# Kernel tuning notes

Measured on AMD Instinct MI355X. Metric: run time of the kernel, lower is better.

Reference implementation:

```python
import jax, jax.numpy as jnp
import numpy as np

L = 28          # layers
D = 1024        # hidden
HQ = 16         # query heads
HKV = 8         # kv heads
HD = 128        # head dim
DFF = 3072      # mlp intermediate
Q = 512         # prefill length (= end_step, past_kv_len = 0)
EPS = 1e-6


def setup_inputs() -> dict:
    key = jax.random.key(0)
    ks = jax.random.split(key, 12)
    s = 0.02
    hidden_states = jax.random.normal(ks[0], (1, Q, D), jnp.float32)
    # RoPE tables (concatenated-halves layout, base 1e6 as in Qwen3)
    pos = jnp.arange(Q, dtype=jnp.float32)
    inv_freq = 1.0 / (1e6 ** (jnp.arange(0, HD, 2, dtype=jnp.float32) / HD))
    freqs = pos[:, None] * inv_freq[None, :]              # [Q, HD/2]
    emb = jnp.concatenate([freqs, freqs], axis=-1)        # [Q, HD]
    position_cos = jnp.cos(emb)[None]                     # [1, Q, HD]
    position_sin = jnp.sin(emb)[None]
    # causal mask: 0 where key_pos <= query_pos else -1e9 ; [1,1,Q,Q]
    i = jnp.arange(Q)
    attention_mask = jnp.where(i[None, :] <= i[:, None], 0.0, -1e9).astype(jnp.float32)[None, None]
    # stacked per-layer weights (torch Linear y = x @ W^T stored here as [in,out])
    Wq = jax.random.normal(ks[1], (L, D, HQ * HD), jnp.float32) * s
    Wk = jax.random.normal(ks[2], (L, D, HKV * HD), jnp.float32) * s
    Wv = jax.random.normal(ks[3], (L, D, HKV * HD), jnp.float32) * s
    Wo = jax.random.normal(ks[4], (L, HQ * HD, D), jnp.float32) * s
    Wg = jax.random.normal(ks[5], (L, D, DFF), jnp.float32) * s
    Wu = jax.random.normal(ks[6], (L, D, DFF), jnp.float32) * s
    Wd = jax.random.normal(ks[7], (L, DFF, D), jnp.float32) * s
    ln1 = jnp.ones((L, D), jnp.float32)
    ln2 = jnp.ones((L, D), jnp.float32)
    qn = jnp.ones((L, HD), jnp.float32)
    kn = jnp.ones((L, HD), jnp.float32)
    return {"hidden_states": hidden_states, "position_cos": position_cos,
            "position_sin": position_sin, "attention_mask": attention_mask,
            "Wq": Wq, "Wk": Wk, "Wv": Wv, "Wo": Wo, "Wg": Wg, "Wu": Wu, "Wd": Wd,
            "ln1": ln1, "ln2": ln2, "qn": qn, "kn": kn}


def rmsnorm(x, w):
    return x * jax.lax.rsqrt(jnp.mean(x * x, axis=-1, keepdims=True) + EPS) * w


def rotate_half(x):
    x1, x2 = jnp.split(x, 2, axis=-1)
    return jnp.concatenate([-x2, x1], axis=-1)


def reference(hidden_states, position_cos, position_sin, attention_mask,
              Wq, Wk, Wv, Wo, Wg, Wu, Wd, ln1, ln2, qn, kn):
    q_len = hidden_states.shape[1]
    scale = 1.0 / np.sqrt(HD)
    cos = position_cos[:, None]   # [1,1,Q,HD] broadcast over heads
    sin = position_sin[:, None]

    def layer(h, p):
        wq, wk, wv, wo, wg, wu, wd, l1, l2, qw, kw = p
        x = rmsnorm(h, l1)
        q = (x @ wq).reshape(1, q_len, HQ, HD).transpose(0, 2, 1, 3)   # [1,HQ,Q,HD]
        k = (x @ wk).reshape(1, q_len, HKV, HD).transpose(0, 2, 1, 3)  # [1,HKV,Q,HD]
        v = (x @ wv).reshape(1, q_len, HKV, HD).transpose(0, 2, 1, 3)
        q = rmsnorm(q, qw)
        k = rmsnorm(k, kw)
        q = q * cos + rotate_half(q) * sin
        k = k * cos + rotate_half(k) * sin
        # fp16 KV-cache round trip (faithful to k.half() store / .float() load)
        k = k.astype(jnp.float16).astype(jnp.float32)
        v = v.astype(jnp.float16).astype(jnp.float32)
        # GQA: repeat kv heads
        k = jnp.repeat(k, HQ // HKV, axis=1)
        v = jnp.repeat(v, HQ // HKV, axis=1)
        scores = jnp.einsum('bhqd,bhkd->bhqk', q, k) * scale + attention_mask
        probs = jax.nn.softmax(scores, axis=-1)
        attn = jnp.einsum('bhqk,bhkd->bhqd', probs, v)
        attn = attn.transpose(0, 2, 1, 3).reshape(1, q_len, HQ * HD)
        h = h + attn @ wo
        y = rmsnorm(h, l2)
        h = h + (jax.nn.silu(y @ wg) * (y @ wu)) @ wd
        return h, None

    params = (Wq, Wk, Wv, Wo, Wg, Wu, Wd, ln1, ln2, qn, kn)
    out, _ = jax.lax.scan(layer, hidden_states, params)
    return out
```

## Files before the change

### kernel.cpp

```cpp
#include <hip/hip_runtime.h>
#include <stdint.h>


typedef __bf16 bf16_t;
typedef _Float16 f16_t;
typedef __bf16 bf16x8 __attribute__((ext_vector_type(8)));
typedef __bf16 bf16x4 __attribute__((ext_vector_type(4)));
typedef _Float16 f16x8 __attribute__((ext_vector_type(8)));
typedef float f32x4 __attribute__((ext_vector_type(4)));

#define SEQ 512
#define HD 128

#define IMG_QKV 0ull
#define IMG_WO  8388608ull
#define IMG_GU  12582912ull
#define IMG_WD  25165824ull
#define IMG_LAYER_BYTES 31457280ull

typedef const __attribute__((address_space(1))) uint32_t as1_u32;
typedef __attribute__((address_space(3))) uint32_t as3_u32;

__device__ __forceinline__ void gload16(const void* g, void* l) {
    __builtin_amdgcn_global_load_lds((as1_u32*)g, (as3_u32*)l, 16, 0, 0);
}

#define WAITV12 asm volatile("s_waitcnt vmcnt(12)" ::: "memory")
#define WAITV6  asm volatile("s_waitcnt vmcnt(6)" ::: "memory")
#define WAITV0  asm volatile("s_waitcnt vmcnt(0)" ::: "memory")

__device__ __forceinline__ size_t aoff(int row, int col, int ldak) {
    return (((size_t)((row >> 6) * ldak + (col >> 6))) << 13) +
           ((size_t)(row & 63) << 7) +
           (size_t)((((col & 63) << 1)) ^ ((row & 7) << 4));
}

__global__ __launch_bounds__(256) void k_copy(const float* __restrict__ src,
                                              float* __restrict__ dst)
{
    size_t i = ((size_t)blockIdx.x * 256 + threadIdx.x) * 4;
    *(float4*)(dst + i) = *(const float4*)(src + i);
}

__device__ __forceinline__ void conv_tile(
    int b, int lay,
    const float* __restrict__ Wq, const float* __restrict__ Wk,
    const float* __restrict__ Wv, const float* __restrict__ Wo,
    const float* __restrict__ Wg, const float* __restrict__ Wu,
    const float* __restrict__ Wd, char* __restrict__ ib, void* smemv)
{
    const float* wq = Wq + (size_t)lay * 1024 * 2048;
    const float* wk = Wk + (size_t)lay * 1024 * 1024;
    const float* wv = Wv + (size_t)lay * 1024 * 1024;
    const float* wo = Wo + (size_t)lay * 2048 * 1024;
    const float* wg = Wg + (size_t)lay * 1024 * 3072;
    const float* wu = Wu + (size_t)lay * 1024 * 3072;
    const float* wd = Wd + (size_t)lay * 3072 * 1024;

    const float* src = nullptr;
    int ldbw = 0, n, kt, guMode = 0;
    size_t dstoff;
    if (b < 1024) {
        n = b >> 4; kt = b & 15;
        int C0 = n * 64;
        if (C0 < 2048)      { src = wq + C0;          ldbw = 2048; }
        else if (C0 < 3072) { src = wk + (C0 - 2048); ldbw = 1024; }
        else                { src = wv + (C0 - 3072); ldbw = 1024; }
        src += (size_t)(kt * 64) * ldbw;
        dstoff = IMG_QKV + (size_t)b * 8192;
    } else if (b < 1536) {
        int b2 = b - 1024; n = b2 >> 5; kt = b2 & 31;
        src = wo + (size_t)(kt * 64) * 1024 + n * 64; ldbw = 1024;
        dstoff = IMG_WO + (size_t)b2 * 8192;
    } else if (b < 3072) {
        int b3 = b - 1536; n = b3 >> 4; kt = b3 & 15;
        guMode = 1; ldbw = 3072;
        dstoff = IMG_GU + (size_t)b3 * 8192;
    } else {
        int b4 = b - 3072; n = b4 / 48; kt = b4 % 48;
        src = wd + (size_t)(kt * 64) * 1024 + n * 64; ldbw = 1024;
        dstoff = IMG_WD + (size_t)b4 * 8192;
    }

    float (*T)[68] = (float (*)[68])smemv;
    int tid = threadIdx.x;
    if (!guMode) {
#pragma unroll
        for (int it = 0; it < 4; ++it) {
            int idx = it * 256 + tid;
            int kk = idx >> 4, seg = idx & 15;
            *(float4*)&T[kk][seg * 4] = *(const float4*)(src + (size_t)kk * ldbw + seg * 4);
        }
    } else {
        const float* wg_ = wg + (size_t)(kt * 64) * 3072;
        const float* wu_ = wu + (size_t)(kt * 64) * 3072;
#pragma unroll
        for (int it = 0; it < 4; ++it) {
            int idx = it * 256 + tid;
            int kk = idx >> 4, seg = idx & 15;
            int nl = seg * 4;
            int colc = n * 32 + ((nl >> 5) & 1) * 16 + (nl & 15);
            const float* s2 = (((nl >> 4) & 1) ? wu_ : wg_) + (size_t)kk * 3072 + colc;
            *(float4*)&T[kk][nl] = *(const float4*)s2;
        }
    }
    __syncthreads();
    char* dst = ib + dstoff;
#pragma unroll
    for (int it = 0; it < 2; ++it) {
        int kg = tid & 7;
        int nrow = it * 32 + (tid >> 3);
        bf16x8 o;
#pragma unroll
        for (int j = 0; j < 8; ++j) o[j] = (bf16_t)T[kg * 8 + j][nrow];
        *(bf16x8*)(dst + nrow * 128 + ((kg * 16) ^ ((nrow & 7) << 4))) = o;
    }
}

__global__ __launch_bounds__(256) void k_conv(
    int lay,
    const float* __restrict__ Wq, const float* __restrict__ Wk,
    const float* __restrict__ Wv, const float* __restrict__ Wo,
    const float* __restrict__ Wg, const float* __restrict__ Wu,
    const float* __restrict__ Wd, char* __restrict__ img)
{
    __shared__ __align__(16) char smem[17408];
    conv_tile(blockIdx.x, lay, Wq, Wk, Wv, Wo, Wg, Wu, Wd, img, smem);
}

__global__ __launch_bounds__(256) void k_rms(
    float* __restrict__ h, const bf16_t* __restrict__ parts, int nparts,
    const float* __restrict__ w, char* __restrict__ ximg)
{
    int t = blockIdx.x, tid = threadIdx.x;
    size_t base = (size_t)t * 1024 + tid * 4;
    float4 v = *(const float4*)(h + base);
    for (int p = 0; p < nparts; ++p) {
        bf16x4 a = *(const bf16x4*)(parts + (size_t)p * 524288 + base);
        v.x += (float)a[0]; v.y += (float)a[1]; v.z += (float)a[2]; v.w += (float)a[3];
    }
    if (nparts) *(float4*)(h + base) = v;
    float ss = v.x * v.x + v.y * v.y + v.z * v.z + v.w * v.w;
#pragma unroll
    for (int m = 1; m < 64; m <<= 1) ss += __shfl_xor(ss, m);
    __shared__ float red[4];
    if ((tid & 63) == 0) red[tid >> 6] = ss;
    __syncthreads();
    float tot = (red[0] + red[1]) + (red[2] + red[3]);
    float sc = rsqrtf(tot * (1.0f / 1024.0f) + 1e-6f);
    float4 wv4 = *(const float4*)(w + tid * 4);
    bf16x4 o;
    o[0] = (bf16_t)(v.x * sc * wv4.x);
    o[1] = (bf16_t)(v.y * sc * wv4.y);
    o[2] = (bf16_t)(v.z * sc * wv4.z);
    o[3] = (bf16_t)(v.w * sc * wv4.w);
    *(bf16x4*)(ximg + aoff(t, tid * 4, 16)) = o;
}

__global__ __launch_bounds__(256) void k_finalize(
    const float* __restrict__ h, const bf16_t* __restrict__ parts,
    float* __restrict__ out)
{
    size_t base = ((size_t)blockIdx.x * 256 + threadIdx.x) * 4;
    float4 v = *(const float4*)(h + base);
#pragma unroll
    for (int p = 0; p < 4; ++p) {
        bf16x4 a = *(const bf16x4*)(parts + (size_t)p * 524288 + base);
        v.x += (float)a[0]; v.y += (float)a[1]; v.z += (float)a[2]; v.w += (float)a[3];
    }
    *(float4*)(out + base) = v;
}

template <int NBN, int SPLITK, int LDAK>
__device__ __forceinline__ void gemm_loop(
    const char* __restrict__ Aimg, const char* __restrict__ Bimg,
    char* smem, int f, f32x4 (&acc)[2][4], int& bmO, int& bnO, int& sO)
{
    const int steps = LDAK / SPLITK;
    int bm = f / (NBN * SPLITK);
    int r = f % (NBN * SPLITK);
    int s = r / NBN;
    int bn = r % NBN;
    int k0d = s * steps;
    bmO = bm; bnO = bn; sO = s;

    int tid = threadIdx.x;
    int wv = tid >> 6, l = tid & 63, lg = l >> 4, lr = l & 15;
    int wr = wv >> 1, wc = wv & 1;

#pragma unroll
    for (int i = 0; i < 2; ++i)
#pragma unroll
        for (int j = 0; j < 4; ++j) { f32x4 z = {0.f, 0.f, 0.f, 0.f}; acc[i][j] = z; }

    auto stage = [&](int buf, int kt) {
        const char* ab = Aimg + ((size_t)(bm * LDAK + k0d + kt)) * 8192;
        const char* b0 = Bimg + ((size_t)((2 * bn) * LDAK + k0d + kt)) * 8192;
        const char* b1 = Bimg + ((size_t)((2 * bn + 1) * LDAK + k0d + kt)) * 8192;
        char* al = smem + buf * 24576;
        char* bl = al + 8192;
#pragma unroll
        for (int u = 0; u < 2; ++u) {
            int off = (wv * 2 + u) * 1024;
            gload16(ab + off + l * 16, al + off);
        }
#pragma unroll
        for (int u = 0; u < 4; ++u) {
            int off = (wv * 4 + u) * 1024;
            const char* src = (off < 8192) ? (b0 + off) : (b1 + off - 8192);
            gload16(src + l * 16, bl + off);
        }
    };
    auto compute = [&](int buf) {
        const char* as = smem + buf * 24576;
        const char* bs = as + 8192 + wc * 8192;
        __builtin_amdgcn_s_setprio(1);
#pragma unroll
        for (int c = 0; c < 2; ++c) {
            int co = (c * 64 + lg * 16) ^ ((lr & 7) << 4);
            bf16x8 af[2], bf[4];
#pragma unroll
            for (int i = 0; i < 2; ++i)
                af[i] = *(const bf16x8*)(as + (wr * 32 + i * 16 + lr) * 128 + co);
#pragma unroll
            for (int j = 0; j < 4; ++j)
                bf[j] = *(const bf16x8*)(bs + (j * 16 + lr) * 128 + co);
#pragma unroll
            for (int i = 0; i < 2; ++i)
#pragma unroll
                for (int j = 0; j < 4; ++j)
                    acc[i][j] = __builtin_amdgcn_mfma_f32_16x16x32_bf16(
                        af[i], bf[j], acc[i][j], 0, 0, 0);
        }
        __builtin_amdgcn_s_setprio(0);
    };

    stage(0, 0);
    stage(1, 1);
    int buf = 0;
    for (int kt = 0; kt < steps; ++kt) {
        if (kt + 2 < steps)      { stage((kt + 2) % 3, kt + 2); WAITV12; }
        else if (kt + 1 < steps) { WAITV6; }
        else                     { WAITV0; }
        __builtin_amdgcn_sched_barrier(0);
        __builtin_amdgcn_s_barrier();
        __builtin_amdgcn_sched_barrier(0);
        compute(buf);
        __builtin_amdgcn_s_barrier();
        buf = (buf == 2) ? 0 : buf + 1;
    }
}

__global__ __launch_bounds__(256) void g_qkvf(
    const char* __restrict__ Aimg, const char* __restrict__ Bimg,
    const float* __restrict__ cosb, const float* __restrict__ sinb,
    const float* __restrict__ qw, const float* __restrict__ kw,
    f16_t* __restrict__ qf, f16_t* __restrict__ kf, f16_t* __restrict__ vT,
    const float* Wq, const float* Wk, const float* Wv, const float* Wo,
    const float* Wg, const float* Wu, const float* Wd,
    int lnext, char* __restrict__ imgnext)
{
    __shared__ __align__(128) char smem[73728];
    if (blockIdx.x >= 256) {
        conv_tile(blockIdx.x - 256, lnext, Wq, Wk, Wv, Wo, Wg, Wu, Wd, imgnext, smem);
        return;
    }
    f32x4 acc[2][4];
    int bm, bn, s;
    gemm_loop<32, 1, 16>(Aimg, Bimg, smem, blockIdx.x, acc, bm, bn, s);

    int tid = threadIdx.x;
    int wv = tid >> 6, l = tid & 63, lg = l >> 4, lr = l & 15;
    int wr = wv >> 1, wc = wv & 1;
    float (*X)[132] = (float (*)[132])smem;
    __syncthreads();
#pragma unroll
    for (int i = 0; i < 2; ++i)
#pragma unroll
        for (int j = 0; j < 4; ++j)
#pragma unroll
            for (int ii = 0; ii < 4; ++ii)
                X[wr * 32 + i * 16 + lg * 4 + ii][wc * 64 + j * 16 + lr] = acc[i][j][ii];
    __syncthreads();

    int t0 = bm * 64;
    if (bn < 24) {
        bool isq = bn < 16;
        int slot = isq ? bn : bn - 16;
        const float* wn = isq ? qw : kw;
        int r = tid >> 2, part = tid & 3;
        float ss = 0.f;
#pragma unroll
        for (int c = 0; c < 32; ++c) { float v = X[r][part * 32 + c]; ss += v * v; }
        ss += __shfl_xor(ss, 1);
        ss += __shfl_xor(ss, 2);
        float sc = rsqrtf(ss * (1.0f / 128.0f) + 1e-6f);
        int t = t0 + r;
        int d0 = part * 16;
        float o1v[16], o2v[16];
#pragma unroll
        for (int c = 0; c < 16; ++c) {
            int d = d0 + c;
            float xv1 = X[r][d] * sc * wn[d];
            float xv2 = X[r][d + 64] * sc * wn[d + 64];
            o1v[c] = xv1 * cosb[t * HD + d] - xv2 * sinb[t * HD + d];
            o2v[c] = xv2 * cosb[t * HD + d + 64] + xv1 * sinb[t * HD + d + 64];
        }
        f16x8 w0, w1, w2, w3;
#pragma unroll
        for (int c = 0; c < 8; ++c) {
            w0[c] = (f16_t)o1v[c];     w1[c] = (f16_t)o1v[8 + c];
            w2[c] = (f16_t)o2v[c];     w3[c] = (f16_t)o2v[8 + c];
        }
        f16_t* o = (isq ? qf : kf) + ((size_t)slot * SEQ + t) * HD;
        *(f16x8*)(o + d0) = w0;
        *(f16x8*)(o + d0 + 8) = w1;
        *(f16x8*)(o + d0 + 64) = w2;
        *(f16x8*)(o + d0 + 72) = w3;
    } else {
        int kvh = bn - 24;
#pragma unroll
        for (int it = 0; it < 4; ++it) {
            int task = it * 256 + tid;
            int d = task >> 3, seg = task & 7;
            f16x8 o;
#pragma unroll
            for (int j = 0; j < 8; ++j) o[j] = (f16_t)X[seg * 8 + j][d];
            *(f16x8*)(vT + ((size_t)kvh * HD + d) * SEQ + t0 + seg * 8) = o;
        }
    }
}

__global__ __launch_bounds__(256) void g_wo(
    const char* A, const char* B, bf16_t* parts,
    const float* Wq, const float* Wk, const float* Wv, const float* Wo,
    const float* Wg, const float* Wu, const float* Wd,
    int lnext, char* imgnext)
{
    __shared__ __align__(128) char smem[73728];
    if (blockIdx.x >= 256) {
        conv_tile(blockIdx.x - 256 + 960, lnext, Wq, Wk, Wv, Wo, Wg, Wu, Wd, imgnext, smem);
        return;
    }
    f32x4 acc[2][4];
    int bm, bn, s;
    gemm_loop<8, 4, 32>(A, B, smem, blockIdx.x, acc, bm, bn, s);
    int tid = threadIdx.x;
    int wv = tid >> 6, l = tid & 63, lg = l >> 4, lr = l & 15;
    int wr = wv >> 1, wc = wv & 1;
    bf16_t* P = parts + (size_t)s * 524288;
#pragma unroll
    for (int i = 0; i < 2; ++i)
#pragma unroll
        for (int j = 0; j < 4; ++j)
#pragma unroll
            for (int ii = 0; ii < 4; ++ii) {
                int row = bm * 64 + wr * 32 + i * 16 + lg * 4 + ii;
                int col = bn * 128 + wc * 64 + j * 16 + lr;
                P[(size_t)row * 1024 + col] = (bf16_t)acc[i][j][ii];
            }
}

__global__ __launch_bounds__(256) void g_gu(
    const char* A, const char* B, char* mimg,
    const float* Wq, const float* Wk, const float* Wv, const float* Wo,
    const float* Wg, const float* Wu, const float* Wd,
    int lnext, char* imgnext)
{
    __shared__ __align__(128) char smem[73728];
    if (blockIdx.x >= 384) {
        conv_tile(blockIdx.x - 384 + 1920, lnext, Wq, Wk, Wv, Wo, Wg, Wu, Wd, imgnext, smem);
        return;
    }
    f32x4 acc[2][4];
    int bm, bn, s;
    gemm_loop<48, 1, 16>(A, B, smem, blockIdx.x, acc, bm, bn, s);
    int tid = threadIdx.x;
    int wv = tid >> 6, l = tid & 63, lg = l >> 4, lr = l & 15;
    int wr = wv >> 1, wc = wv & 1;
#pragma unroll
    for (int i = 0; i < 2; ++i)
#pragma unroll
        for (int jp = 0; jp < 2; ++jp)
#pragma unroll
            for (int ii = 0; ii < 4; ++ii) {
                int row = bm * 64 + wr * 32 + i * 16 + lg * 4 + ii;
                int col = (bn * 2 + wc) * 32 + jp * 16 + lr;
                float gv = acc[i][2 * jp][ii];
                float uv = acc[i][2 * jp + 1][ii];
                float val = gv / (1.f + __expf(-gv)) * uv;
                *(bf16_t*)(mimg + aoff(row, col, 48)) = (bf16_t)val;
            }
}

__global__ __launch_bounds__(256) void k_wdc(
    const char* A, const char* B, bf16_t* parts,
    const float* Wq, const float* Wk, const float* Wv, const float* Wo,
    const float* Wg, const float* Wu, const float* Wd,
    int lnext, char* imgnext)
{
    __shared__ __align__(128) char smem[73728];
    int b = blockIdx.x;
    if (b >= 256) {
        conv_tile(b - 256 + 2880, lnext, Wq, Wk, Wv, Wo, Wg, Wu, Wd, imgnext, smem);
        return;
    }
    f32x4 acc[2][4];
    int bm, bn, s;
    gemm_loop<8, 4, 48>(A, B, smem, b, acc, bm, bn, s);
    int tid = threadIdx.x;
    int wv = tid >> 6, l = tid & 63, lg = l >> 4, lr = l & 15;
    int wr = wv >> 1, wc = wv & 1;
    bf16_t* P = parts + (size_t)s * 524288;
#pragma unroll
    for (int i = 0; i < 2; ++i)
#pragma unroll
        for (int j = 0; j < 4; ++j)
#pragma unroll
            for (int ii = 0; ii < 4; ++ii) {
                int row = bm * 64 + wr * 32 + i * 16 + lg * 4 + ii;
                int col = bn * 128 + wc * 64 + j * 16 + lr;
                P[(size_t)row * 1024 + col] = (bf16_t)acc[i][j][ii];
            }
}

__global__ __launch_bounds__(128) void k_attn(
    const f16_t* __restrict__ qf, const f16_t* __restrict__ kf,
    const f16_t* __restrict__ vT, char* __restrict__ attimg)
{
    int h = blockIdx.x >> 4, qb = 15 - (blockIdx.x & 15);
    int kvh = h >> 1;
    __shared__ f16_t Kt[64][136];
    __shared__ f16_t Vt[128][72];
    __shared__ f16_t Pl[2][16][72];
    int tid = threadIdx.x;
    int wv = tid >> 6, l = tid & 63, lg = l >> 4, lr = l & 15;
    int q0 = qb * 32;
    int qrow = q0 + wv * 16;

    f16x8 aq[4];
    const f16_t* qp = qf + ((size_t)h * SEQ + qrow + lr) * HD;
#pragma unroll
    for (int c = 0; c < 4; ++c) aq[c] = *(const f16x8*)(qp + c * 32 + lg * 8);

    f32x4 accv[8];
#pragma unroll
    for (int df = 0; df < 8; ++df) { f32x4 z = {0.f, 0.f, 0.f, 0.f}; accv[df] = z; }
    float mrun[4], lrun[4];
#pragma unroll
    for (int ii = 0; ii < 4; ++ii) { mrun[ii] = -3e38f; lrun[ii] = 0.f; }

    int ktiles = (q0 + 32 + 63) >> 6;
    for (int kt = 0; kt < ktiles; ++kt) {
        int kt0 = kt * 64;
        __syncthreads();
#pragma unroll
        for (int it = 0; it < 8; ++it) {
            int idx = it * 128 + tid;
            int r = idx >> 4, seg = idx & 15;
            *(int4*)&Kt[r][seg * 8] =
                *(const int4*)(kf + ((size_t)kvh * SEQ + kt0 + r) * HD + seg * 8);
        }
#pragma unroll
        for (int it = 0; it < 8; ++it) {
            int idx = it * 128 + tid;
            int r = idx >> 3, seg = idx & 7;
            *(int4*)&Vt[r][seg * 8] =
                *(const int4*)(vT + ((size_t)kvh * HD + r) * SEQ + kt0 + seg * 8);
        }
        __syncthreads();

        f32x4 s[4];
#pragma unroll
        for (int nf = 0; nf < 4; ++nf) {
            f32x4 a = {0.f, 0.f, 0.f, 0.f};
#pragma unroll
            for (int c = 0; c < 4; ++c) {
                f16x8 bk = *(const f16x8*)&Kt[nf * 16 + lr][c * 32 + lg * 8];
                a = __builtin_amdgcn_mfma_f32_16x16x32_f16(aq[c], bk, a, 0, 0, 0);
            }
            s[nf] = a;
        }
        const float scale = 0.08838834764831845f;
        float tmax[4] = {-3e38f, -3e38f, -3e38f, -3e38f};
#pragma unroll
        for (int nf = 0; nf < 4; ++nf) {
            int ktg = kt0 + nf * 16 + lr;
#pragma unroll
            for (int ii = 0; ii < 4; ++ii) {
                int qg = qrow + lg * 4 + ii;
                float vv = s[nf][ii] * scale;
                vv = (ktg <= qg) ? vv : -1e30f;
                s[nf][ii] = vv;
                tmax[ii] = fmaxf(tmax[ii], vv);
            }
        }
#pragma unroll
        for (int m = 1; m < 16; m <<= 1)
#pragma unroll
            for (int ii = 0; ii < 4; ++ii)
                tmax[ii] = fmaxf(tmax[ii], __shfl_xor(tmax[ii], m));
        float corr[4];
#pragma unroll
        for (int ii = 0; ii < 4; ++ii) {
            float mnew = fmaxf(mrun[ii], tmax[ii]);
            corr[ii] = __expf(mrun[ii] - mnew);
            mrun[ii] = mnew;
        }
        float tsum[4] = {0.f, 0.f, 0.f, 0.f};
#pragma unroll
        for (int nf = 0; nf < 4; ++nf)
#pragma unroll
            for (int ii = 0; ii < 4; ++ii) {
                float pp = __expf(s[nf][ii] - mrun[ii]);
                s[nf][ii] = pp;
                tsum[ii] += pp;
            }
#pragma unroll
        for (int m = 1; m < 16; m <<= 1)
#pragma unroll
            for (int ii = 0; ii < 4; ++ii) tsum[ii] += __shfl_xor(tsum[ii], m);
#pragma unroll
        for (int ii = 0; ii < 4; ++ii) lrun[ii] = lrun[ii] * corr[ii] + tsum[ii];
#pragma unroll
        for (int df = 0; df < 8; ++df)
#pragma unroll
            for (int ii = 0; ii < 4; ++ii) accv[df][ii] *= corr[ii];
#pragma unroll
        for (int nf = 0; nf < 4; ++nf)
#pragma unroll
            for (int ii = 0; ii < 4; ++ii)
                Pl[wv][lg * 4 + ii][nf * 16 + lr] = (f16_t)s[nf][ii];
        __syncthreads();
#pragma unroll
        for (int c = 0; c < 2; ++c) {
            f16x8 ap = *(const f16x8*)&Pl[wv][lr][c * 32 + lg * 8];
#pragma unroll
            for (int df = 0; df < 8; ++df) {
                f16x8 bv = *(const f16x8*)&Vt[df * 16 + lr][c * 32 + lg * 8];
                accv[df] = __builtin_amdgcn_mfma_f32_16x16x32_f16(ap, bv, accv[df], 0, 0, 0);
            }
        }
    }
#pragma unroll
    for (int df = 0; df < 8; ++df)
#pragma unroll
        for (int ii = 0; ii < 4; ++ii) {
            int qg = qrow + lg * 4 + ii;
            int col = h * HD + df * 16 + lr;
            *(bf16_t*)(attimg + aoff(qg, col, 32)) =
                (bf16_t)(accv[df][ii] / lrun[ii]);
        }
}

extern "C" void kernel_launch(void* const* d_in, const int* in_sizes, int n_in,
                              void* d_out, int out_size, void* d_ws, size_t ws_size,
                              hipStream_t stream)
{
    const float* hin  = (const float*)d_in[0];
    const float* cosb = (const float*)d_in[1];
    const float* sinb = (const float*)d_in[2];
    const float* Wq = (const float*)d_in[4];
    const float* Wk = (const float*)d_in[5];
    const float* Wv = (const float*)d_in[6];
    const float* Wo = (const float*)d_in[7];
    const float* Wg = (const float*)d_in[8];
    const float* Wu = (const float*)d_in[9];
    const float* Wd = (const float*)d_in[10];
    const float* Ln1 = (const float*)d_in[11];
    const float* Ln2 = (const float*)d_in[12];
    const float* Qn = (const float*)d_in[13];
    const float* Kn = (const float*)d_in[14];

    char* p = (char*)d_ws;
    auto alloc = [&](size_t bytes) { char* r = p; p += bytes; return r; };
    float*  h     = (float*)alloc(2097152);
    bf16_t* parts = (bf16_t*)alloc(4194304);
    char*   ximg  = alloc(1048576);
    char*   yimg  = alloc(1048576);
    char*   attimg= alloc(2097152);
    char*   mimg  = alloc(3145728);
    f16_t*  qf    = (f16_t*)alloc(2097152);
    f16_t*  kf    = (f16_t*)alloc(1048576);
    f16_t*  vT    = (f16_t*)alloc(1048576);
    char*   imgA  = alloc(IMG_LAYER_BYTES);
    size_t fixed = (size_t)(imgA + IMG_LAYER_BYTES - (char*)d_ws);
    bool pp = ws_size >= fixed + IMG_LAYER_BYTES;
    char* imgB = pp ? alloc(IMG_LAYER_BYTES) : imgA;

    k_copy<<<512, 256, 0, stream>>>(hin, h);
    k_conv<<<3840, 256, 0, stream>>>(0, Wq, Wk, Wv, Wo, Wg, Wu, Wd, imgA);

    for (int l = 0; l < 28; ++l) {
        char* img  = (l & 1) ? imgB : imgA;
        char* imgn = (l & 1) ? imgA : imgB;
        bool cv = pp && (l < 27);
        int ln = l + 1;

        k_rms<<<512, 256, 0, stream>>>(h, parts, l == 0 ? 0 : 4,
                                       Ln1 + (size_t)l * 1024, ximg);
        g_qkvf<<<cv ? 1216 : 256, 256, 0, stream>>>(
            ximg, img + IMG_QKV, cosb, sinb,
            Qn + (size_t)l * 128, Kn + (size_t)l * 128, qf, kf, vT,
            Wq, Wk, Wv, Wo, Wg, Wu, Wd, ln, imgn);
        k_attn<<<256, 128, 0, stream>>>(qf, kf, vT, attimg);
        g_wo<<<cv ? 1216 : 256, 256, 0, stream>>>(
            attimg, img + IMG_WO, parts,
            Wq, Wk, Wv, Wo, Wg, Wu, Wd, ln, imgn);
        k_rms<<<512, 256, 0, stream>>>(h, parts, 4, Ln2 + (size_t)l * 1024, yimg);
        g_gu<<<cv ? 1344 : 384, 256, 0, stream>>>(
            yimg, img + IMG_GU, mimg,
            Wq, Wk, Wv, Wo, Wg, Wu, Wd, ln, imgn);
        k_wdc<<<cv ? 1216 : 256, 256, 0, stream>>>(
            mimg, img + IMG_WD, parts,
            Wq, Wk, Wv, Wo, Wg, Wu, Wd, ln, imgn);
        if (!pp && l < 27)
            k_conv<<<3840, 256, 0, stream>>>(ln, Wq, Wk, Wv, Wo, Wg, Wu, Wd, imgA);
    }
    k_finalize<<<512, 256, 0, stream>>>(h, parts, (float*)d_out);
}
```

Before: 2.343 ms.

## Fold RMSNorm into weights and GEMM epilogues, drop split-K and rms kernels

The RMSNorm weights ln1/ln2 are now folded into the bf16 weight images during conversion. The per-row inverse RMS scale is applied after the GEMM: it is only applied to V and to gate/up, since the q/k head norms make the row scale cancel. The separate k_rms and k_finalize kernels and the bf16 split-K partial buffers are removed. The Wo and Wd GEMMs run without split-K and add directly into the fp32 residual h, also writing the next layer's bf16 activation image. This cuts two launches per layer and the partial-sum traffic, but leaves only 64 GEMM blocks for Wo/Wd with longer K loops. It also recomputes row norms redundantly in every gate/up block and feeds unnormalized bf16 activations into the GEMMs.

```diff
diff --git a/kernel.cpp b/kernel.cpp
--- a/kernel.cpp
+++ b/kernel.cpp
@@ -36,10 +36,16 @@
 }
 
 __global__ __launch_bounds__(256) void k_copy(const float* __restrict__ src,
-                                              float* __restrict__ dst)
-{
-    size_t i = ((size_t)blockIdx.x * 256 + threadIdx.x) * 4;
-    *(float4*)(dst + i) = *(const float4*)(src + i);
+                                              float* __restrict__ h,
+                                              char* __restrict__ ximg)
+{
+    int t = blockIdx.x, tid = threadIdx.x;
+    size_t base = (size_t)t * 1024 + tid * 4;
+    float4 v = *(const float4*)(src + base);
+    *(float4*)(h + base) = v;
+    bf16x4 o;
+    o[0] = (bf16_t)v.x; o[1] = (bf16_t)v.y; o[2] = (bf16_t)v.z; o[3] = (bf16_t)v.w;
+    *(bf16x4*)(ximg + aoff(t, tid * 4, 16)) = o;
 }
 
 __device__ __forceinline__ void conv_tile(
@@ -47,7 +53,9 @@
     const float* __restrict__ Wq, const float* __restrict__ Wk,
     const float* __restrict__ Wv, const float* __restrict__ Wo,
     const float* __restrict__ Wg, const float* __restrict__ Wu,
-    const float* __restrict__ Wd, char* __restrict__ ib, void* smemv)
+    const float* __restrict__ Wd,
+    const float* __restrict__ Ln1, const float* __restrict__ Ln2,
+    char* __restrict__ ib, void* smemv)
 {
     const float* wq = Wq + (size_t)lay * 1024 * 2048;
     const float* wk = Wk + (size_t)lay * 1024 * 1024;
@@ -58,6 +66,7 @@
     const float* wd = Wd + (size_t)lay * 3072 * 1024;
 
     const float* src = nullptr;
+    const float* lnp = nullptr;
     int ldbw = 0, n, kt, guMode = 0;
     size_t dstoff;
     if (b < 1024) {
@@ -67,6 +76,7 @@
         else if (C0 < 3072) { src = wk + (C0 - 2048); ldbw = 1024; }
         else                { src = wv + (C0 - 3072); ldbw = 1024; }
         src += (size_t)(kt * 64) * ldbw;
+        lnp = Ln1 + (size_t)lay * 1024 + kt * 64;
         dstoff = IMG_QKV + (size_t)b * 8192;
     } else if (b < 1536) {
         int b2 = b - 1024; n = b2 >> 5; kt = b2 & 31;
@@ -75,6 +85,7 @@
     } else if (b < 3072) {
         int b3 = b - 1536; n = b3 >> 4; kt = b3 & 15;
         guMode = 1; ldbw = 3072;
+        lnp = Ln2 + (size_t)lay * 1024 + kt * 64;
         dstoff = IMG_GU + (size_t)b3 * 8192;
     } else {
         int b4 = b - 3072; n = b4 / 48; kt = b4 % 48;
@@ -89,7 +100,12 @@
         for (int it = 0; it < 4; ++it) {
             int idx = it * 256 + tid;
             int kk = idx >> 4, seg = idx & 15;
-            *(float4*)&T[kk][seg * 4] = *(const float4*)(src + (size_t)kk * ldbw + seg * 4);
+            float4 vv = *(const float4*)(src + (size_t)kk * ldbw + seg * 4);
+            if (lnp) {
+                float s = lnp[kk];
+                vv.x *= s; vv.y *= s; vv.z *= s; vv.w *= s;
+            }
+            *(float4*)&T[kk][seg * 4] = vv;
         }
     } else {
         const float* wg_ = wg + (size_t)(kt * 64) * 3072;
@@ -101,7 +117,10 @@
             int nl = seg * 4;
             int colc = n * 32 + ((nl >> 5) & 1) * 16 + (nl & 15);
             const float* s2 = (((nl >> 4) & 1) ? wu_ : wg_) + (size_t)kk * 3072 + colc;
-            *(float4*)&T[kk][nl] = *(const float4*)s2;
+            float4 vv = *(const float4*)s2;
+            float s = lnp[kk];
+            vv.x *= s; vv.y *= s; vv.z *= s; vv.w *= s;
+            *(float4*)&T[kk][nl] = vv;
         }
     }
     __syncthreads();
@@ -122,67 +141,24 @@
     const float* __restrict__ Wq, const float* __restrict__ Wk,
     const float* __restrict__ Wv, const float* __restrict__ Wo,
     const float* __restrict__ Wg, const float* __restrict__ Wu,
-    const float* __restrict__ Wd, char* __restrict__ img)
+    const float* __restrict__ Wd,
+    const float* __restrict__ Ln1, const float* __restrict__ Ln2,
+    char* __restrict__ img)
 {
     __shared__ __align__(16) char smem[17408];
-    conv_tile(blockIdx.x, lay, Wq, Wk, Wv, Wo, Wg, Wu, Wd, img, smem);
-}
-
-__global__ __launch_bounds__(256) void k_rms(
-    float* __restrict__ h, const bf16_t* __restrict__ parts, int nparts,
-    const float* __restrict__ w, char* __restrict__ ximg)
-{
-    int t = blockIdx.x, tid = threadIdx.x;
-    size_t base = (size_t)t * 1024 + tid * 4;
-    float4 v = *(const float4*)(h + base);
-    for (int p = 0; p < nparts; ++p) {
-        bf16x4 a = *(const bf16x4*)(parts + (size_t)p * 524288 + base);
-        v.x += (float)a[0]; v.y += (float)a[1]; v.z += (float)a[2]; v.w += (float)a[3];
-    }
-    if (nparts) *(float4*)(h + base) = v;
-    float ss = v.x * v.x + v.y * v.y + v.z * v.z + v.w * v.w;
-#pragma unroll
-    for (int m = 1; m < 64; m <<= 1) ss += __shfl_xor(ss, m);
-    __shared__ float red[4];
-    if ((tid & 63) == 0) red[tid >> 6] = ss;
-    __syncthreads();
-    float tot = (red[0] + red[1]) + (red[2] + red[3]);
-    float sc = rsqrtf(tot * (1.0f / 1024.0f) + 1e-6f);
-    float4 wv4 = *(const float4*)(w + tid * 4);
-    bf16x4 o;
-    o[0] = (bf16_t)(v.x * sc * wv4.x);
-    o[1] = (bf16_t)(v.y * sc * wv4.y);
-    o[2] = (bf16_t)(v.z * sc * wv4.z);
-    o[3] = (bf16_t)(v.w * sc * wv4.w);
-    *(bf16x4*)(ximg + aoff(t, tid * 4, 16)) = o;
-}
-
-__global__ __launch_bounds__(256) void k_finalize(
-    const float* __restrict__ h, const bf16_t* __restrict__ parts,
-    float* __restrict__ out)
-{
-    size_t base = ((size_t)blockIdx.x * 256 + threadIdx.x) * 4;
-    float4 v = *(const float4*)(h + base);
-#pragma unroll
-    for (int p = 0; p < 4; ++p) {
-        bf16x4 a = *(const bf16x4*)(parts + (size_t)p * 524288 + base);
-        v.x += (float)a[0]; v.y += (float)a[1]; v.z += (float)a[2]; v.w += (float)a[3];
-    }
-    *(float4*)(out + base) = v;
+    conv_tile(blockIdx.x, lay, Wq, Wk, Wv, Wo, Wg, Wu, Wd, Ln1, Ln2, img, smem);
 }
 
 template <int NBN, int SPLITK, int LDAK>
 __device__ __forceinline__ void gemm_loop(
     const char* __restrict__ Aimg, const char* __restrict__ Bimg,
-    char* smem, int f, f32x4 (&acc)[2][4], int& bmO, int& bnO, int& sO)
+    char* smem, int f, f32x4 (&acc)[2][4], int& bmO, int& bnO)
 {
     const int steps = LDAK / SPLITK;
     int bm = f / (NBN * SPLITK);
     int r = f % (NBN * SPLITK);
-    int s = r / NBN;
     int bn = r % NBN;
-    int k0d = s * steps;
-    bmO = bm; bnO = bn; sO = s;
+    bmO = bm; bnO = bn;
 
     int tid = threadIdx.x;
     int wv = tid >> 6, l = tid & 63, lg = l >> 4, lr = l & 15;
@@ -194,9 +170,9 @@
         for (int j = 0; j < 4; ++j) { f32x4 z = {0.f, 0.f, 0.f, 0.f}; acc[i][j] = z; }
 
     auto stage = [&](int buf, int kt) {
-        const char* ab = Aimg + ((size_t)(bm * LDAK + k0d + kt)) * 8192;
-        const char* b0 = Bimg + ((size_t)((2 * bn) * LDAK + k0d + kt)) * 8192;
-        const char* b1 = Bimg + ((size_t)((2 * bn + 1) * LDAK + k0d + kt)) * 8192;
+        const char* ab = Aimg + ((size_t)(bm * LDAK + kt)) * 8192;
+        const char* b0 = Bimg + ((size_t)((2 * bn) * LDAK + kt)) * 8192;
+        const char* b1 = Bimg + ((size_t)((2 * bn + 1) * LDAK + kt)) * 8192;
         char* al = smem + buf * 24576;
         char* bl = al + 8192;
 #pragma unroll
@@ -251,28 +227,49 @@
     }
 }
 
+__device__ __forceinline__ void row_scales(const float* __restrict__ h,
+                                           int t0, float* sl)
+{
+    int tid = threadIdx.x;
+    int r = tid >> 2, q4 = tid & 3;
+    const float* hr = h + (size_t)(t0 + r) * 1024 + q4 * 256;
+    float ss = 0.f;
+#pragma unroll
+    for (int c = 0; c < 64; ++c) {
+        float4 v = *(const float4*)(hr + c * 4);
+        ss += v.x * v.x + v.y * v.y + v.z * v.z + v.w * v.w;
+    }
+    ss += __shfl_xor(ss, 1);
+    ss += __shfl_xor(ss, 2);
+    if (q4 == 0) sl[r] = rsqrtf(ss * (1.0f / 1024.0f) + 1e-6f);
+}
+
 __global__ __launch_bounds__(256) void g_qkvf(
     const char* __restrict__ Aimg, const char* __restrict__ Bimg,
     const float* __restrict__ cosb, const float* __restrict__ sinb,
     const float* __restrict__ qw, const float* __restrict__ kw,
+    const float* __restrict__ h,
     f16_t* __restrict__ qf, f16_t* __restrict__ kf, f16_t* __restrict__ vT,
     const float* Wq, const float* Wk, const float* Wv, const float* Wo,
     const float* Wg, const float* Wu, const float* Wd,
+    const float* Ln1, const float* Ln2,
     int lnext, char* __restrict__ imgnext)
 {
     __shared__ __align__(128) char smem[73728];
     if (blockIdx.x >= 256) {
-        conv_tile(blockIdx.x - 256, lnext, Wq, Wk, Wv, Wo, Wg, Wu, Wd, imgnext, smem);
+        conv_tile(blockIdx.x - 256, lnext, Wq, Wk, Wv, Wo, Wg, Wu, Wd,
+                  Ln1, Ln2, imgnext, smem);
         return;
     }
     f32x4 acc[2][4];
-    int bm, bn, s;
-    gemm_loop<32, 1, 16>(Aimg, Bimg, smem, blockIdx.x, acc, bm, bn, s);
+    int bm, bn;
+    gemm_loop<32, 1, 16>(Aimg, Bimg, smem, blockIdx.x, acc, bm, bn);
 
     int tid = threadIdx.x;
     int wv = tid >> 6, l = tid & 63, lg = l >> 4, lr = l & 15;
     int wr = wv >> 1, wc = wv & 1;
     float (*X)[132] = (float (*)[132])smem;
+    float* sl = (float*)(smem + 64 * 132 * 4 + 128);
     __syncthreads();
 #pragma unroll
     for (int i = 0; i < 2; ++i)
@@ -281,9 +278,10 @@
 #pragma unroll
             for (int ii = 0; ii < 4; ++ii)
                 X[wr * 32 + i * 16 + lg * 4 + ii][wc * 64 + j * 16 + lr] = acc[i][j][ii];
+    int t0 = bm * 64;
+    if (bn >= 24) row_scales(h, t0, sl);
     __syncthreads();
 
-    int t0 = bm * 64;
     if (bn < 24) {
         bool isq = bn < 16;
         int slot = isq ? bn : bn - 16;
@@ -325,30 +323,33 @@
             int d = task >> 3, seg = task & 7;
             f16x8 o;
 #pragma unroll
-            for (int j = 0; j < 8; ++j) o[j] = (f16_t)X[seg * 8 + j][d];
+            for (int j = 0; j < 8; ++j)
+                o[j] = (f16_t)(X[seg * 8 + j][d] * sl[seg * 8 + j]);
             *(f16x8*)(vT + ((size_t)kvh * HD + d) * SEQ + t0 + seg * 8) = o;
         }
     }
 }
 
 __global__ __launch_bounds__(256) void g_wo(
-    const char* A, const char* B, bf16_t* parts,
+    const char* __restrict__ A, const char* __restrict__ B,
+    float* __restrict__ h, char* __restrict__ yimg,
     const float* Wq, const float* Wk, const float* Wv, const float* Wo,
     const float* Wg, const float* Wu, const float* Wd,
+    const float* Ln1, const float* Ln2,
     int lnext, char* imgnext)
 {
     __shared__ __align__(128) char smem[73728];
-    if (blockIdx.x >= 256) {
-        conv_tile(blockIdx.x - 256 + 960, lnext, Wq, Wk, Wv, Wo, Wg, Wu, Wd, imgnext, smem);
+    if (blockIdx.x >= 64) {
+        conv_tile(blockIdx.x - 64 + 960, lnext, Wq, Wk, Wv, Wo, Wg, Wu, Wd,
+                  Ln1, Ln2, imgnext, smem);
         return;
     }
     f32x4 acc[2][4];
-    int bm, bn, s;
-    gemm_loop<8, 4, 32>(A, B, smem, blockIdx.x, acc, bm, bn, s);
+    int bm, bn;
+    gemm_loop<8, 1, 32>(A, B, smem, blockIdx.x, acc, bm, bn);
     int tid = threadIdx.x;
     int wv = tid >> 6, l = tid & 63, lg = l >> 4, lr = l & 15;
     int wr = wv >> 1, wc = wv & 1;
-    bf16_t* P = parts + (size_t)s * 524288;
 #pragma unroll
     for (int i = 0; i < 2; ++i)
 #pragma unroll
@@ -357,61 +358,72 @@
             for (int ii = 0; ii < 4; ++ii) {
                 int row = bm * 64 + wr * 32 + i * 16 + lg * 4 + ii;
                 int col = bn * 128 + wc * 64 + j * 16 + lr;
-                P[(size_t)row * 1024 + col] = (bf16_t)acc[i][j][ii];
+                float hv = h[(size_t)row * 1024 + col] + acc[i][j][ii];
+                h[(size_t)row * 1024 + col] = hv;
+                *(bf16_t*)(yimg + aoff(row, col, 16)) = (bf16_t)hv;
             }
 }
 
 __global__ __launch_bounds__(256) void g_gu(
-    const char* A, const char* B, char* mimg,
+    const char* __restrict__ A, const char* __restrict__ B,
+    const float* __restrict__ h, char* __restrict__ mimg,
     const float* Wq, const float* Wk, const float* Wv, const float* Wo,
     const float* Wg, const float* Wu, const float* Wd,
+    const float* Ln1, const float* Ln2,
     int lnext, char* imgnext)
 {
     __shared__ __align__(128) char smem[73728];
     if (blockIdx.x >= 384) {
-        conv_tile(blockIdx.x - 384 + 1920, lnext, Wq, Wk, Wv, Wo, Wg, Wu, Wd, imgnext, smem);
+        conv_tile(blockIdx.x - 384 + 1920, lnext, Wq, Wk, Wv, Wo, Wg, Wu, Wd,
+                  Ln1, Ln2, imgnext, smem);
         return;
     }
     f32x4 acc[2][4];
-    int bm, bn, s;
-    gemm_loop<48, 1, 16>(A, B, smem, blockIdx.x, acc, bm, bn, s);
+    int bm, bn;
+    gemm_loop<48, 1, 16>(A, B, smem, blockIdx.x, acc, bm, bn);
     int tid = threadIdx.x;
     int wv = tid >> 6, l = tid & 63, lg = l >> 4, lr = l & 15;
     int wr = wv >> 1, wc = wv & 1;
+    float* sarr = (float*)smem;
+    row_scales(h, bm * 64, sarr);
+    __syncthreads();
 #pragma unroll
     for (int i = 0; i < 2; ++i)
 #pragma unroll
         for (int jp = 0; jp < 2; ++jp)
 #pragma unroll
             for (int ii = 0; ii < 4; ++ii) {
-                int row = bm * 64 + wr * 32 + i * 16 + lg * 4 + ii;
+                int lrow = wr * 32 + i * 16 + lg * 4 + ii;
+                int row = bm * 64 + lrow;
                 int col = (bn * 2 + wc) * 32 + jp * 16 + lr;
-                float gv = acc[i][2 * jp][ii];
-                float uv = acc[i][2 * jp + 1][ii];
+                float s = sarr[lrow];
+                float gv = acc[i][2 * jp][ii] * s;
+                float uv = acc[i][2 * jp + 1][ii] * s;
                 float val = gv / (1.f + __expf(-gv)) * uv;
                 *(bf16_t*)(mimg + aoff(row, col, 48)) = (bf16_t)val;
             }
 }
 
-__global__ __launch_bounds__(256) void k_wdc(
-    const char* A, const char* B, bf16_t* parts,
+__global__ __launch_bounds__(256) void g_wd(
+    const char* __restrict__ A, const char* __restrict__ B,
+    float* __restrict__ h, char* __restrict__ ximg, float* __restrict__ fout,
     const float* Wq, const float* Wk, const float* Wv, const float* Wo,
     const float* Wg, const float* Wu, const float* Wd,
+    const float* Ln1, const float* Ln2,
     int lnext, char* imgnext)
 {
     __shared__ __align__(128) char smem[73728];
-    int b = blockIdx.x;
-    if (b >= 256) {
-        conv_tile(b - 256 + 2880, lnext, Wq, Wk, Wv, Wo, Wg, Wu, Wd, imgnext, smem);
+    if (blockIdx.x >= 64) {
+        conv_tile(blockIdx.x - 64 + 2880, lnext, Wq, Wk, Wv, Wo, Wg, Wu, Wd,
+                  Ln1, Ln2, imgnext, smem);
         return;
     }
     f32x4 acc[2][4];
-    int bm, bn, s;
-    gemm_loop<8, 4, 48>(A, B, smem, b, acc, bm, bn, s);
+    int bm, bn;
+    gemm_loop<8, 1, 48>(A, B, smem, blockIdx.x, acc, bm, bn);
     int tid = threadIdx.x;
     int wv = tid >> 6, l = tid & 63, lg = l >> 4, lr = l & 15;
     int wr = wv >> 1, wc = wv & 1;
-    bf16_t* P = parts + (size_t)s * 524288;
 #pragma unroll
     for (int i = 0; i < 2; ++i)
 #pragma unroll
@@ -420,7 +432,13 @@
             for (int ii = 0; ii < 4; ++ii) {
                 int row = bm * 64 + wr * 32 + i * 16 + lg * 4 + ii;
                 int col = bn * 128 + wc * 64 + j * 16 + lr;
-                P[(size_t)row * 1024 + col] = (bf16_t)acc[i][j][ii];
+                float hv = h[(size_t)row * 1024 + col] + acc[i][j][ii];
+                if (fout) {
+                    fout[(size_t)row * 1024 + col] = hv;
+                } else {
+                    h[(size_t)row * 1024 + col] = hv;
+                    *(bf16_t*)(ximg + aoff(row, col, 16)) = (bf16_t)hv;
+                }
             }
 }
 
@@ -575,7 +593,6 @@
     char* p = (char*)d_ws;
     auto alloc = [&](size_t bytes) { char* r = p; p += bytes; return r; };
     float*  h     = (float*)alloc(2097152);
-    bf16_t* parts = (bf16_t*)alloc(4194304);
     char*   ximg  = alloc(1048576);
     char*   yimg  = alloc(1048576);
     char*   attimg= alloc(2097152);
@@ -588,34 +605,35 @@
     bool pp = ws_size >= fixed + IMG_LAYER_BYTES;
     char* imgB = pp ? alloc(IMG_LAYER_BYTES) : imgA;
 
-    k_copy<<<512, 256, 0, stream>>>(hin, h);
-    k_conv<<<3840, 256, 0, stream>>>(0, Wq, Wk, Wv, Wo, Wg, Wu, Wd, imgA);
+    k_copy<<<512, 256, 0, stream>>>(hin, h, ximg);
+    if (pp)
+        k_conv<<<3840, 256, 0, stream>>>(0, Wq, Wk, Wv, Wo, Wg, Wu, Wd,
+                                         Ln1, Ln2, imgA);
 
     for (int l = 0; l < 28; ++l) {
-        char* img  = (l & 1) ? imgB : imgA;
-        char* imgn = (l & 1) ? imgA : imgB;
+        char* img  = pp ? ((l & 1) ? imgB : imgA) : imgA;
+        char* imgn = pp ? ((l & 1) ? imgA : imgB) : imgA;
         bool cv = pp && (l < 27);
         int ln = l + 1;
 
-        k_rms<<<512, 256, 0, stream>>>(h, parts, l == 0 ? 0 : 4,
-                                       Ln1 + (size_t)l * 1024, ximg);
+        if (!pp)
+            k_conv<<<3840, 256, 0, stream>>>(l, Wq, Wk, Wv, Wo, Wg, Wu, Wd,
+                                             Ln1, Ln2, imgA);
+
         g_qkvf<<<cv ? 1216 : 256, 256, 0, stream>>>(
             ximg, img + IMG_QKV, cosb, sinb,
-            Qn + (size_t)l * 128, Kn + (size_t)l * 128, qf, kf, vT,
-            Wq, Wk, Wv, Wo, Wg, Wu, Wd, ln, imgn);
+            Qn + (size_t)l * 128, Kn + (size_t)l * 128, h, qf, kf, vT,
+            Wq, Wk, Wv, Wo, Wg, Wu, Wd, Ln1, Ln2, ln, imgn);
         k_attn<<<256, 128, 0, stream>>>(qf, kf, vT, attimg);
-        g_wo<<<cv ? 1216 : 256, 256, 0, stream>>>(
-            attimg, img + IMG_WO, parts,
-            Wq, Wk, Wv, Wo, Wg, Wu, Wd, ln, imgn);
-        k_rms<<<512, 256, 0, stream>>>(h, parts, 4, Ln2 + (size_t)l * 1024, yimg);
+        g_wo<<<cv ? 1024 : 64, 256, 0, stream>>>(
+            attimg, img + IMG_WO, h, yimg,
+            Wq, Wk, Wv, Wo, Wg, Wu, Wd, Ln1, Ln2, ln, imgn);
         g_gu<<<cv ? 1344 : 384, 256, 0, stream>>>(
-            yimg, img + IMG_GU, mimg,
-            Wq, Wk, Wv, Wo, Wg, Wu, Wd, ln, imgn);
-        k_wdc<<<cv ? 1216 : 256, 256, 0, stream>>>(
-            mimg, img + IMG_WD, parts,
-            Wq, Wk, Wv, Wo, Wg, Wu, Wd, ln, imgn);
-        if (!pp && l < 27)
-            k_conv<<<3840, 256, 0, stream>>>(ln, Wq, Wk, Wv, Wo, Wg, Wu, Wd, imgA);
-    }
-    k_finalize<<<512, 256, 0, stream>>>(h, parts, (float*)d_out);
-}
+            yimg, img + IMG_GU, h, mimg,
+            Wq, Wk, Wv, Wo, Wg, Wu, Wd, Ln1, Ln2, ln, imgn);
+        g_wd<<<cv ? 1024 : 64, 256, 0, stream>>>(
+            mimg, img + IMG_WD, h, ximg,
+            (l == 27) ? (float*)d_out : nullptr,
+            Wq, Wk, Wv, Wo, Wg, Wu, Wd, Ln1, Ln2, ln, imgn);
+    }
+}
```

Result: slower. 3.630 ms (+54.9%).

## Fuse residual-add RMSNorm into split-K GEMM epilogues via last-block atomic counters

Applied to the files above, without the earlier changes.

Removes the standalone k_rms and k_finalize launches. Each split-K partial block of the Wo and Wd GEMMs now bumps a per-row-tile atomic counter, and the last block to finish sums the four bf16 partials into the residual and performs RMSNorm for the next stage, or writes the final output. The goal is to cut two kernel launches per layer and the extra global round trip over the residual. The cost is that the normalization now runs in only 8 blocks with serialized per-thread loops over 256 columns, plus atomics and fences.

```diff
diff --git a/kernel.cpp b/kernel.cpp
--- a/kernel.cpp
+++ b/kernel.cpp
@@ -35,11 +35,35 @@
            (size_t)((((col & 63) << 1)) ^ ((row & 7) << 4));
 }
 
-__global__ __launch_bounds__(256) void k_copy(const float* __restrict__ src,
-                                              float* __restrict__ dst)
-{
-    size_t i = ((size_t)blockIdx.x * 256 + threadIdx.x) * 4;
-    *(float4*)(dst + i) = *(const float4*)(src + i);
+#define CNT_U32 14336
+__global__ __launch_bounds__(256) void k_zero(uint32_t* c) {
+    int i = blockIdx.x * 256 + threadIdx.x;
+    if (i < CNT_U32) c[i] = 0;
+}
+
+__global__ __launch_bounds__(256) void k_start(
+    const float* __restrict__ hin, float* __restrict__ h,
+    const float* __restrict__ w, char* __restrict__ ximg)
+{
+    int t = blockIdx.x, tid = threadIdx.x;
+    size_t base = (size_t)t * 1024 + tid * 4;
+    float4 v = *(const float4*)(hin + base);
+    *(float4*)(h + base) = v;
+    float ss = v.x * v.x + v.y * v.y + v.z * v.z + v.w * v.w;
+#pragma unroll
+    for (int m = 1; m < 64; m <<= 1) ss += __shfl_xor(ss, m);
+    __shared__ float red[4];
+    if ((tid & 63) == 0) red[tid >> 6] = ss;
+    __syncthreads();
+    float tot = (red[0] + red[1]) + (red[2] + red[3]);
+    float sc = rsqrtf(tot * (1.0f / 1024.0f) + 1e-6f);
+    float4 wv4 = *(const float4*)(w + tid * 4);
+    bf16x4 o;
+    o[0] = (bf16_t)(v.x * sc * wv4.x);
+    o[1] = (bf16_t)(v.y * sc * wv4.y);
+    o[2] = (bf16_t)(v.z * sc * wv4.z);
+    o[3] = (bf16_t)(v.w * sc * wv4.w);
+    *(bf16x4*)(ximg + aoff(t, tid * 4, 16)) = o;
 }
 
 __device__ __forceinline__ void conv_tile(
@@ -128,49 +152,6 @@
     conv_tile(blockIdx.x, lay, Wq, Wk, Wv, Wo, Wg, Wu, Wd, img, smem);
 }
 
-__global__ __launch_bounds__(256) void k_rms(
-    float* __restrict__ h, const bf16_t* __restrict__ parts, int nparts,
-    const float* __restrict__ w, char* __restrict__ ximg)
-{
-    int t = blockIdx.x, tid = threadIdx.x;
-    size_t base = (size_t)t * 1024 + tid * 4;
-    float4 v = *(const float4*)(h + base);
-    for (int p = 0; p < nparts; ++p) {
-        bf16x4 a = *(const bf16x4*)(parts + (size_t)p * 524288 + base);
-        v.x += (float)a[0]; v.y += (float)a[1]; v.z += (float)a[2]; v.w += (float)a[3];
-    }
-    if (nparts) *(float4*)(h + base) = v;
-    float ss = v.x * v.x + v.y * v.y + v.z * v.z + v.w * v.w;
-#pragma unroll
-    for (int m = 1; m < 64; m <<= 1) ss += __shfl_xor(ss, m);
-    __shared__ float red[4];
-    if ((tid & 63) == 0) red[tid >> 6] = ss;
-    __syncthreads();
-    float tot = (red[0] + red[1]) + (red[2] + red[3]);
-    float sc = rsqrtf(tot * (1.0f / 1024.0f) + 1e-6f);
-    float4 wv4 = *(const float4*)(w + tid * 4);
-    bf16x4 o;
-    o[0] = (bf16_t)(v.x * sc * wv4.x);
-    o[1] = (bf16_t)(v.y * sc * wv4.y);
-    o[2] = (bf16_t)(v.z * sc * wv4.z);
-    o[3] = (bf16_t)(v.w * sc * wv4.w);
-    *(bf16x4*)(ximg + aoff(t, tid * 4, 16)) = o;
-}
-
-__global__ __launch_bounds__(256) void k_finalize(
-    const float* __restrict__ h, const bf16_t* __restrict__ parts,
-    float* __restrict__ out)
-{
-    size_t base = ((size_t)blockIdx.x * 256 + threadIdx.x) * 4;
-    float4 v = *(const float4*)(h + base);
-#pragma unroll
-    for (int p = 0; p < 4; ++p) {
-        bf16x4 a = *(const bf16x4*)(parts + (size_t)p * 524288 + base);
-        v.x += (float)a[0]; v.y += (float)a[1]; v.z += (float)a[2]; v.w += (float)a[3];
-    }
-    *(float4*)(out + base) = v;
-}
-
 template <int NBN, int SPLITK, int LDAK>
 __device__ __forceinline__ void gemm_loop(
     const char* __restrict__ Aimg, const char* __restrict__ Bimg,
@@ -251,6 +232,81 @@
     }
 }
 
+__device__ __forceinline__ void rms_fixup(
+    int bm, float* __restrict__ h, const bf16_t* __restrict__ parts,
+    const float* __restrict__ w, char* __restrict__ img,
+    float* __restrict__ dout)
+{
+    int tid = threadIdx.x;
+    int r = bm * 64 + (tid >> 2), q4 = tid & 3;
+    float* hr = h + (size_t)r * 1024 + q4 * 256;
+    const bf16_t* pr = parts + (size_t)r * 1024 + q4 * 256;
+    float ss = 0.f;
+    for (int c = 0; c < 64; ++c) {
+        float4 v = *(const float4*)(hr + c * 4);
+#pragma unroll
+        for (int p = 0; p < 4; ++p) {
+            bf16x4 a = *(const bf16x4*)(pr + (size_t)p * 524288 + c * 4);
+            v.x += (float)a[0]; v.y += (float)a[1];
+            v.z += (float)a[2]; v.w += (float)a[3];
+        }
+        if (dout) *(float4*)(dout + (size_t)r * 1024 + q4 * 256 + c * 4) = v;
+        else      *(float4*)(hr + c * 4) = v;
+        ss += v.x * v.x + v.y * v.y + v.z * v.z + v.w * v.w;
+    }
+    if (dout) return;
+    ss += __shfl_xor(ss, 1);
+    ss += __shfl_xor(ss, 2);
+    float sc = rsqrtf(ss * (1.0f / 1024.0f) + 1e-6f);
+    for (int c = 0; c < 64; ++c) {
+        float4 v = *(const float4*)(hr + c * 4);
+        int col = q4 * 256 + c * 4;
+        bf16x4 o;
+        o[0] = (bf16_t)(v.x * sc * w[col]);
+        o[1] = (bf16_t)(v.y * sc * w[col + 1]);
+        o[2] = (bf16_t)(v.z * sc * w[col + 2]);
+        o[3] = (bf16_t)(v.w * sc * w[col + 3]);
+        *(bf16x4*)(img + aoff(r, col, 16)) = o;
+    }
+}
+
+template <int LDAK>
+__device__ __forceinline__ int part_job(
+    int f, const char* A, const char* B, bf16_t* parts, char* smem,
+    uint32_t* cnt, int& bmO)
+{
+    f32x4 acc[2][4];
+    int bm, bn, s;
+    gemm_loop<8, 4, LDAK>(A, B, smem, f, acc, bm, bn, s);
+    bmO = bm;
+    int tid = threadIdx.x;
+    int wv = tid >> 6, l = tid & 63, lg = l >> 4, lr = l & 15;
+    int wr = wv >> 1, wc = wv & 1;
+    bf16_t* P = parts + (size_t)s * 524288;
+#pragma unroll
+    for (int i = 0; i < 2; ++i)
+#pragma unroll
+        for (int j = 0; j < 4; ++j)
+#pragma unroll
+            for (int ii = 0; ii < 4; ++ii) {
+                int row = bm * 64 + wr * 32 + i * 16 + lg * 4 + ii;
+                int col = bn * 128 + wc * 64 + j * 16 + lr;
+                P[(size_t)row * 1024 + col] = (bf16_t)acc[i][j][ii];
+            }
+    __shared__ int lastf;
+    __threadfence();
+    if (tid == 0) {
+        uint32_t old = __hip_atomic_fetch_add(cnt + bm * 32, 1u,
+                                              __ATOMIC_ACQ_REL,
+                                              __HIP_MEMORY_SCOPE_AGENT);
+        lastf = (old == 31u);
+    }
+    __syncthreads();
+    if (!lastf) return 0;
+    __threadfence();
+    return 1;
+}
+
 __global__ __launch_bounds__(256) void g_qkvf(
     const char* __restrict__ Aimg, const char* __restrict__ Bimg,
     const float* __restrict__ cosb, const float* __restrict__ sinb,
@@ -333,6 +389,8 @@
 
 __global__ __launch_bounds__(256) void g_wo(
     const char* A, const char* B, bf16_t* parts,
+    float* __restrict__ h, char* __restrict__ yimg,
+    const float* __restrict__ ln2v, uint32_t* __restrict__ cnt,
     const float* Wq, const float* Wk, const float* Wv, const float* Wo,
     const float* Wg, const float* Wu, const float* Wd,
     int lnext, char* imgnext)
@@ -342,23 +400,9 @@
         conv_tile(blockIdx.x - 256 + 960, lnext, Wq, Wk, Wv, Wo, Wg, Wu, Wd, imgnext, smem);
         return;
     }
-    f32x4 acc[2][4];
-    int bm, bn, s;
-    gemm_loop<8, 4, 32>(A, B, smem, blockIdx.x, acc, bm, bn, s);
-    int tid = threadIdx.x;
-    int wv = tid >> 6, l = tid & 63, lg = l >> 4, lr = l & 15;
-    int wr = wv >> 1, wc = wv & 1;
-    bf16_t* P = parts + (size_t)s * 524288;
-#pragma unroll
-    for (int i = 0; i < 2; ++i)
-#pragma unroll
-        for (int j = 0; j < 4; ++j)
-#pragma unroll
-            for (int ii = 0; ii < 4; ++ii) {
-                int row = bm * 64 + wr * 32 + i * 16 + lg * 4 + ii;
-                int col = bn * 128 + wc * 64 + j * 16 + lr;
-                P[(size_t)row * 1024 + col] = (bf16_t)acc[i][j][ii];
-            }
+    int bm;
+    if (part_job<32>(blockIdx.x, A, B, parts, smem, cnt, bm))
+        rms_fixup(bm, h, parts, ln2v, yimg, nullptr);
 }
 
 __global__ __launch_bounds__(256) void g_gu(
@@ -393,35 +437,23 @@
             }
 }
 
-__global__ __launch_bounds__(256) void k_wdc(
+__global__ __launch_bounds__(256) void g_wd(
     const char* A, const char* B, bf16_t* parts,
+    float* __restrict__ h, char* __restrict__ ximg,
+    const float* __restrict__ ln1n, uint32_t* __restrict__ cnt,
+    float* __restrict__ dout,
     const float* Wq, const float* Wk, const float* Wv, const float* Wo,
     const float* Wg, const float* Wu, const float* Wd,
     int lnext, char* imgnext)
 {
     __shared__ __align__(128) char smem[73728];
-    int b = blockIdx.x;
-    if (b >= 256) {
-        conv_tile(b - 256 + 2880, lnext, Wq, Wk, Wv, Wo, Wg, Wu, Wd, imgnext, smem);
+    if (blockIdx.x >= 256) {
+        conv_tile(blockIdx.x - 256 + 2880, lnext, Wq, Wk, Wv, Wo, Wg, Wu, Wd, imgnext, smem);
         return;
     }
-    f32x4 acc[2][4];
-    int bm, bn, s;
-    gemm_loop<8, 4, 48>(A, B, smem, b, acc, bm, bn, s);
-    int tid = threadIdx.x;
-    int wv = tid >> 6, l = tid & 63, lg = l >> 4, lr = l & 15;
-    int wr = wv >> 1, wc = wv & 1;
-    bf16_t* P = parts + (size_t)s * 524288;
-#pragma unroll
-    for (int i = 0; i < 2; ++i)
-#pragma unroll
-        for (int j = 0; j < 4; ++j)
-#pragma unroll
-            for (int ii = 0; ii < 4; ++ii) {
-                int row = bm * 64 + wr * 32 + i * 16 + lg * 4 + ii;
-                int col = bn * 128 + wc * 64 + j * 16 + lr;
-                P[(size_t)row * 1024 + col] = (bf16_t)acc[i][j][ii];
-            }
+    int bm;
+    if (part_job<48>(blockIdx.x, A, B, parts, smem, cnt, bm))
+        rms_fixup(bm, h, parts, ln1n, ximg, dout);
 }
 
 __global__ __launch_bounds__(128) void k_attn(
@@ -583,39 +615,43 @@
     f16_t*  qf    = (f16_t*)alloc(2097152);
     f16_t*  kf    = (f16_t*)alloc(1048576);
     f16_t*  vT    = (f16_t*)alloc(1048576);
+    uint32_t* cnts= (uint32_t*)alloc(CNT_U32 * 4);
     char*   imgA  = alloc(IMG_LAYER_BYTES);
     size_t fixed = (size_t)(imgA + IMG_LAYER_BYTES - (char*)d_ws);
     bool pp = ws_size >= fixed + IMG_LAYER_BYTES;
     char* imgB = pp ? alloc(IMG_LAYER_BYTES) : imgA;
 
-    k_copy<<<512, 256, 0, stream>>>(hin, h);
+    k_zero<<<(CNT_U32 + 255) / 256, 256, 0, stream>>>(cnts);
+    k_start<<<512, 256, 0, stream>>>(hin, h, Ln1, ximg);
     k_conv<<<3840, 256, 0, stream>>>(0, Wq, Wk, Wv, Wo, Wg, Wu, Wd, imgA);
 
     for (int l = 0; l < 28; ++l) {
-        char* img  = (l & 1) ? imgB : imgA;
-        char* imgn = (l & 1) ? imgA : imgB;
+        char* img  = pp ? ((l & 1) ? imgB : imgA) : imgA;
+        char* imgn = pp ? ((l & 1) ? imgA : imgB) : imgA;
         bool cv = pp && (l < 27);
         int ln = l + 1;
-
-        k_rms<<<512, 256, 0, stream>>>(h, parts, l == 0 ? 0 : 4,
-                                       Ln1 + (size_t)l * 1024, ximg);
+        uint32_t* cwo = cnts + (l * 2 + 0) * 256;
+        uint32_t* cwd = cnts + (l * 2 + 1) * 256;
+
+        if (!pp && l > 0)
+            k_conv<<<3840, 256, 0, stream>>>(l, Wq, Wk, Wv, Wo, Wg, Wu, Wd, imgA);
+
         g_qkvf<<<cv ? 1216 : 256, 256, 0, stream>>>(
             ximg, img + IMG_QKV, cosb, sinb,
             Qn + (size_t)l * 128, Kn + (size_t)l * 128, qf, kf, vT,
             Wq, Wk, Wv, Wo, Wg, Wu, Wd, ln, imgn);
         k_attn<<<256, 128, 0, stream>>>(qf, kf, vT, attimg);
         g_wo<<<cv ? 1216 : 256, 256, 0, stream>>>(
-            attimg, img + IMG_WO, parts,
+            attimg, img + IMG_WO, parts, h, yimg,
+            Ln2 + (size_t)l * 1024, cwo,
             Wq, Wk, Wv, Wo, Wg, Wu, Wd, ln, imgn);
-        k_rms<<<512, 256, 0, stream>>>(h, parts, 4, Ln2 + (size_t)l * 1024, yimg);
         g_gu<<<cv ? 1344 : 384, 256, 0, stream>>>(
             yimg, img + IMG_GU, mimg,
             Wq, Wk, Wv, Wo, Wg, Wu, Wd, ln, imgn);
-        k_wdc<<<cv ? 1216 : 256, 256, 0, stream>>>(
-            mimg, img + IMG_WD, parts,
+        g_wd<<<cv ? 1216 : 256, 256, 0, stream>>>(
+            mimg, img + IMG_WD, parts, h, ximg,
+            Ln1 + (size_t)ln * 1024, cwd,
+            (l == 27) ? (float*)d_out : nullptr,
             Wq, Wk, Wv, Wo, Wg, Wu, Wd, ln, imgn);
-        if (!pp && l < 27)
-            k_conv<<<3840, 256, 0, stream>>>(ln, Wq, Wk, Wv, Wo, Wg, Wu, Wd, imgA);
-    }
-    k_finalize<<<512, 256, 0, stream>>>(h, parts, (float*)d_out);
-}
+    }
+}
```

After: 8.936 ms. 281% more time.
